# Kernel tuning notes

Measured on AMD Instinct MI355X. Metric: run time of the kernel, lower is better.

## Reference

```python
import jax, jax.numpy as jnp
import numpy as np

B, N, D, H, FF = 2, 2048, 768, 12, 3072
HD = D // H
RADIUS = 2.0
COORD_DIM = 3
LN_EPS = 1e-5


def _layernorm(x, g, b):
    m = jnp.mean(x, axis=-1, keepdims=True)
    v = jnp.mean((x - m) ** 2, axis=-1, keepdims=True)
    return (x - m) * jax.lax.rsqrt(v + LN_EPS) * g + b


def setup_inputs() -> dict:
    key = jax.random.key(0)
    ks = jax.random.split(key, 16)
    s = 0.02
    return {
        "x": jax.random.normal(ks[0], (B, N, D), jnp.float32),
        "coords": jax.random.uniform(ks[1], (B, N, COORD_DIM), jnp.float32) * 10.0,
        "w_qkv": jax.random.normal(ks[2], (D, 3 * D), jnp.float32) * s,
        "b_qkv": jnp.zeros((3 * D,), jnp.float32),
        "w_out": jax.random.normal(ks[3], (D, D), jnp.float32) * s,
        "b_out": jnp.zeros((D,), jnp.float32),
        "w_ff1": jax.random.normal(ks[4], (D, FF), jnp.float32) * s,
        "b_ff1": jnp.zeros((FF,), jnp.float32),
        "w_ff2": jax.random.normal(ks[5], (FF, D), jnp.float32) * s,
        "b_ff2": jnp.zeros((D,), jnp.float32),
        "g1": jnp.ones((D,), jnp.float32),
        "beta1": jnp.zeros((D,), jnp.float32),
        "g2": jnp.ones((D,), jnp.float32),
        "beta2": jnp.zeros((D,), jnp.float32),
    }


def reference(x, coords, w_qkv, b_qkv, w_out, b_out, w_ff1, b_ff1,
              w_ff2, b_ff2, g1, beta1, g2, beta2):
    # --- attention sub-block ---
    residual = x
    xn = _layernorm(x, g1, beta1)
    qkv = xn @ w_qkv + b_qkv                       # [B,N,3D]
    qkv = qkv.reshape(B, N, 3, H, HD)
    q, k, v = qkv[:, :, 0], qkv[:, :, 1], qkv[:, :, 2]   # [B,N,H,HD]

    # geometric radius mask: attend only to tokens within Euclidean RADIUS
    d2 = jnp.sum((coords[:, :, None, :] - coords[:, None, :, :]) ** 2, axis=-1)  # [B,N,N]
    mask = d2 <= RADIUS * RADIUS                   # self-distance 0 -> always true

    scores = jnp.einsum("bqhd,bkhd->bhqk", q, k) / jnp.sqrt(jnp.float32(HD))
    scores = jnp.where(mask[:, None, :, :], scores, jnp.float32(-1e9))
    attn = jax.nn.softmax(scores, axis=-1)
    attn_out = jnp.einsum("bhqk,bkhd->bqhd", attn, v).reshape(B, N, D)
    attn_out = attn_out @ w_out + b_out            # dropout=0 (eval)
    x = residual + attn_out

    # --- FFN sub-block ---
    residual = x
    xn = _layernorm(x, g2, beta2)
    h = jax.nn.gelu(xn @ w_ff1 + b_ff1, approximate=False)
    ff_out = h @ w_ff2 + b_ff2
    return residual + ff_out
```

## Files before the change

kernel.cpp:

```cpp
#include <hip/hip_runtime.h>
#include <hip/hip_bf16.h>

typedef unsigned short ushort_t;
typedef __attribute__((ext_vector_type(4))) float f32x4;
typedef __attribute__((ext_vector_type(8))) short s16x8;

#define DEV static __device__ __forceinline__

constexpr int Bb = 2, Nn = 2048, Dd = 768, Hh = 12, FFf = 3072;
constexpr int MTOK = Bb * Nn;
constexpr int QKVN = 3 * Dd;

DEV unsigned short f2bf(float f) {
    union { float f; unsigned int i; } x; x.f = f;
    unsigned int r = x.i + 0x7FFFu + ((x.i >> 16) & 1u);
    return (unsigned short)(r >> 16);
}

DEV void gload16(const void* g, void* l) {
    __builtin_amdgcn_global_load_lds(
        (const __attribute__((address_space(1))) void*)g,
        (__attribute__((address_space(3))) void*)l, 16, 0, 0);
}

DEV int xcd_swz(int lin, int n) {
    return (lin & 7) * (n >> 3) + (lin >> 3);
}

__global__ void k_transpose(const float* __restrict__ in, unsigned short* __restrict__ out,
                            int K, int N) {
    __shared__ float t[32][33];
    int bx = blockIdx.x * 32, by = blockIdx.y * 32;
    int tx = threadIdx.x, ty = threadIdx.y;
#pragma unroll
    for (int i = 0; i < 4; i++)
        t[ty + 8 * i][tx] = in[(size_t)(by + ty + 8 * i) * N + bx + tx];
    __syncthreads();
#pragma unroll
    for (int i = 0; i < 4; i++)
        out[(size_t)(bx + ty + 8 * i) * K + by + tx] = f2bf(t[tx][ty + 8 * i]);
}

__global__ void k_coords(const float* __restrict__ c, float4* __restrict__ out, int n) {
    int i = blockIdx.x * 256 + threadIdx.x;
    if (i < n) out[i] = make_float4(c[3 * i], c[3 * i + 1], c[3 * i + 2], 0.f);
}

DEV int cell_of(float4 c) {
    int cx = (int)(c.x * 0.5f); cx = cx > 4 ? 4 : cx;
    int cy = (int)(c.y * 0.5f); cy = cy > 4 ? 4 : cy;
    int cz = (int)(c.z * 0.5f); cz = cz > 4 ? 4 : cz;
    return (cz * 5 + cy) * 5 + cx;
}

__global__ __launch_bounds__(256) void k_sort(const float4* __restrict__ c4,
                                              int* __restrict__ s2o,
                                              float4* __restrict__ c4s) {
    int b = blockIdx.y;
    int i = blockIdx.x * 4 + (threadIdx.x >> 6);
    int lane = threadIdx.x & 63;
    const float4* cb = c4 + b * Nn;
    float4 ci = cb[i];
    int celli = cell_of(ci);
    int pos = 0;
    for (int it = 0; it < Nn / 64; it++) {
        int j = it * 64 + lane;
        int cj = cell_of(cb[j]);
        bool before = (cj < celli) || (cj == celli && j < i);
        pos += __popcll(__ballot(before));
    }
    if (lane == 0) {
        s2o[b * Nn + pos] = i;
        c4s[b * Nn + pos] = ci;
    }
}

__global__ __launch_bounds__(256) void k_mask(const float4* __restrict__ c4s,
                                              unsigned long long* __restrict__ mb) {
    int qt = blockIdx.x, ks = blockIdx.y, b = blockIdx.z;
    __shared__ float4 ck[256];
    int t = threadIdx.x;
    ck[t] = c4s[b * Nn + ks * 256 + t];
    __syncthreads();
    int r = t >> 2, c = t & 3;
    int q = qt * 64 + r;
    float4 cq = c4s[b * Nn + q];
    unsigned long long w = 0;
#pragma unroll 8
    for (int j = 0; j < 64; j++) {
        float4 k4 = ck[c * 64 + j];
        float dx = __fsub_rn(cq.x, k4.x);
        float dy = __fsub_rn(cq.y, k4.y);
        float dz = __fsub_rn(cq.z, k4.z);
        float d2 = __fadd_rn(__fadd_rn(__fmul_rn(dx, dx), __fmul_rn(dy, dy)),
                             __fmul_rn(dz, dz));
        if (d2 <= 4.0f) w |= 1ull << j;
    }
    mb[((size_t)(b * Nn + q) << 5) + ks * 4 + c] = w;
}

__global__ __launch_bounds__(64) void k_tiles(const unsigned long long* __restrict__ mb,
                                              int* __restrict__ tl) {
    int q64 = blockIdx.x, b = blockIdx.y;
    int lane = threadIdx.x;
    unsigned long long v = 0;
    if (lane < 32) {
        const unsigned long long* base = mb + ((size_t)(b * Nn + q64 * 64) << 5) + lane;
        for (int r = 0; r < 64; r++) v |= base[(size_t)r << 5];
    }
    unsigned long long nz = __ballot(v != 0);
    int idx = __popcll(nz & ((1ull << lane) - 1));
    int* o = tl + (b * 32 + q64) * 33;
    if (v != 0) o[1 + idx] = lane;
    if (lane == 0) o[0] = __popcll(nz);
}

__global__ __launch_bounds__(128) void k_gatherK(const unsigned short* __restrict__ qkv,
                                                 const int* __restrict__ s2o,
                                                 unsigned short* __restrict__ Ksort) {
    int ns = blockIdx.x & (Nn - 1);
    int b = blockIdx.x >> 11;
    int t = threadIdx.x;
    int orig = s2o[b * Nn + ns];
    const s16x8* src = (const s16x8*)(qkv + ((size_t)b * Nn + orig) * QKVN + Dd);
    s16x8* dst = (s16x8*)(Ksort + ((size_t)b * Nn + ns) * Dd);
    if (t < 96) dst[t] = src[t];
}

__global__ __launch_bounds__(256) void k_vt(const unsigned short* __restrict__ qkv,
                                            const int* __restrict__ s2o,
                                            unsigned short* __restrict__ VtT) {
    __shared__ unsigned short Ld[64][72];
    int ns0 = blockIdx.x * 64;
    int bh = blockIdx.y;
    int b = bh / Hh, h = bh % Hh;
    int t = threadIdx.x;
#pragma unroll
    for (int i = 0; i < 2; i++) {
        int item = t + 256 * i;
        int row = item >> 3, ch = (item & 7) * 8;
        int orig = s2o[b * Nn + ns0 + row];
        *(s16x8*)&Ld[row][ch] =
            *(const s16x8*)(qkv + ((size_t)b * Nn + orig) * QKVN + 2 * Dd + h * 64 + ch);
    }
    __syncthreads();
    int vd = (t >> 5) * 8, vkp = (t & 31) * 2;
#pragma unroll
    for (int j = 0; j < 8; j++) {
        unsigned int pack = (unsigned int)Ld[vkp][vd + j] |
                            ((unsigned int)Ld[vkp + 1][vd + j] << 16);
        *(unsigned int*)((char*)VtT +
                         (((size_t)bh * 64 + vd + j) * Nn + ns0 + vkp) * 2) = pack;
    }
}

DEV float wred_sum(float v) {
#pragma unroll
    for (int o = 32; o; o >>= 1) v += __shfl_down(v, o, 64);
    return v;
}

__global__ __launch_bounds__(256) void k_ln(const float* __restrict__ x,
                                            const float* __restrict__ g,
                                            const float* __restrict__ be,
                                            unsigned short* __restrict__ out) {
    int row = blockIdx.x;
    const float* xr = x + (size_t)row * Dd;
    int t = threadIdx.x;
    float v0 = xr[t], v1 = xr[t + 256], v2 = xr[t + 512];
    float s = v0 + v1 + v2;
    float sq = v0 * v0 + v1 * v1 + v2 * v2;
    __shared__ float r1[4], r2[4];
    float ws = wred_sum(s), wq = wred_sum(sq);
    int wid = t >> 6, lane = t & 63;
    if (lane == 0) { r1[wid] = ws; r2[wid] = wq; }
    __syncthreads();
    s = r1[0] + r1[1] + r1[2] + r1[3];
    sq = r2[0] + r2[1] + r2[2] + r2[3];
    float mean = s * (1.f / Dd);
    float var = sq * (1.f / Dd) - mean * mean;
    float rs = rsqrtf(var + 1e-5f);
    unsigned short* orow = out + (size_t)row * Dd;
    orow[t]       = f2bf((v0 - mean) * rs * g[t]       + be[t]);
    orow[t + 256] = f2bf((v1 - mean) * rs * g[t + 256] + be[t + 256]);
    orow[t + 512] = f2bf((v2 - mean) * rs * g[t + 512] + be[t + 512]);
}

#define GEMM_PIPE_LOOP(NT)                                                              \
    stage(0, 0);                                                                        \
    for (int t = 0; t < (NT); t++) {                                                    \
        int cur = t & 1;                                                                \
        if (t + 1 < (NT)) {                                                             \
            stage(cur ^ 1, t + 1);                                                      \
            asm volatile("s_waitcnt vmcnt(4)" ::: "memory");                            \
        } else {                                                                        \
            asm volatile("s_waitcnt vmcnt(0)" ::: "memory");                            \
        }                                                                               \
        __builtin_amdgcn_sched_barrier(0);                                              \
        __builtin_amdgcn_s_barrier();                                                   \
        const unsigned short* Ab = As[cur];                                             \
        const unsigned short* Bbp = Bs[cur];                                            \
        s16x8 af[4], bfr[4];                                                            \
        _Pragma("unroll")                                                               \
        for (int i = 0; i < 4; i++) {                                                   \
            af[i]  = *(const s16x8*)&Ab[(wr * 64 + i * 16 + lr) * 32 + lg * 8];         \
            bfr[i] = *(const s16x8*)&Bbp[(wc * 64 + i * 16 + lr) * 32 + lg * 8];        \
        }                                                                               \
        __builtin_amdgcn_s_setprio(1);                                                  \
        _Pragma("unroll")                                                               \
        for (int mi = 0; mi < 4; mi++)                                                  \
            _Pragma("unroll")                                                           \
            for (int ni = 0; ni < 4; ni++)                                              \
                acc[mi][ni] = __builtin_amdgcn_mfma_f32_16x16x32_bf16(                  \
                    af[mi], bfr[ni], acc[mi][ni], 0, 0, 0);                             \
        __builtin_amdgcn_s_setprio(0);                                                  \
        __builtin_amdgcn_s_barrier();                                                   \
    }

template <int EPI>
__global__ __launch_bounds__(256) void k_gemm(const unsigned short* __restrict__ A,
                                              const unsigned short* __restrict__ Bt,
                                              const float* __restrict__ bias,
                                              const float* __restrict__ res,
                                              void* __restrict__ outp,
                                              int M, int N, int K) {
    constexpr int BM = 128, BN = 128, BK = 32;
    __shared__ unsigned short As[2][BM * BK];
    __shared__ unsigned short Bs[2][BN * BK];
    int NB = N >> 7;
    int id = xcd_swz(blockIdx.x, gridDim.x);
    int m0 = (id / NB) * BM, n0 = (id % NB) * BN;
    int t = threadIdx.x;
    int wid = t >> 6, lane = t & 63;
    int wr = wid >> 1, wc = wid & 1;
    int lg = lane >> 4, lr = lane & 15;
    f32x4 acc[4][4] = {};

    int srow = wid * 32 + (lane >> 2);
    int scol = (lane & 3) * 8;
    const unsigned short* Ag = A + (size_t)(m0 + srow) * K + scol;
    const unsigned short* Bg = Bt + (size_t)(n0 + srow) * K + scol;

    auto stage = [&](int buf, int kt) {
        int k0 = kt * BK;
        char* Al = (char*)As[buf] + wid * 2048;
        char* Bl = (char*)Bs[buf] + wid * 2048;
        gload16(Ag + k0, Al);
        gload16(Ag + k0 + (size_t)16 * K, Al + 1024);
        gload16(Bg + k0, Bl);
        gload16(Bg + k0 + (size_t)16 * K, Bl + 1024);
    };
    int nt = K / BK;
    GEMM_PIPE_LOOP(nt)

    int mrow = m0 + wr * 64;
    int ncol = n0 + wc * 64;
#pragma unroll
    for (int mi = 0; mi < 4; mi++) {
#pragma unroll
        for (int ni = 0; ni < 4; ni++) {
            int nn = ncol + ni * 16 + lr;
            float bs = bias[nn];
#pragma unroll
            for (int r = 0; r < 4; r++) {
                int mm = mrow + mi * 16 + lg * 4 + r;
                float v = acc[mi][ni][r] + bs;
                if (EPI == 1) {
                    v = 0.5f * v * (1.f + erff(v * 0.70710678118f));
                    ((unsigned short*)outp)[(size_t)mm * N + nn] = f2bf(v);
                } else if (EPI == 2) {
                    v += res[(size_t)mm * N + nn];
                    ((float*)outp)[(size_t)mm * N + nn] = v;
                } else {
                    ((unsigned short*)outp)[(size_t)mm * N + nn] = f2bf(v);
                }
            }
        }
    }
}

template <int SPLIT>
__global__ __launch_bounds__(256) void k_gemm_sk(const unsigned short* __restrict__ A,
                                                 const unsigned short* __restrict__ Bt,
                                                 float* __restrict__ part,
                                                 int M, int N, int K) {
    constexpr int BM = 128, BN = 128, BK = 32;
    __shared__ unsigned short As[2][BM * BK];
    __shared__ unsigned short Bs[2][BN * BK];
    int NB = N >> 7, MB = M >> 7;
    int id = xcd_swz(blockIdx.x, gridDim.x);
    int nb = id % NB;
    int mbk = (id / NB) % MB;
    int kz = id / (NB * MB);
    int m0 = mbk * BM, n0 = nb * BN;
    int Kc = K / SPLIT, kb = kz * (Kc / BK);
    int t = threadIdx.x;
    int wid = t >> 6, lane = t & 63;
    int wr = wid >> 1, wc = wid & 1;
    int lg = lane >> 4, lr = lane & 15;
    f32x4 acc[4][4] = {};

    int srow = wid * 32 + (lane >> 2);
    int scol = (lane & 3) * 8;
    const unsigned short* Ag = A + (size_t)(m0 + srow) * K + scol;
    const unsigned short* Bg = Bt + (size_t)(n0 + srow) * K + scol;

    auto stage = [&](int buf, int kt) {
        int k0 = (kb + kt) * BK;
        char* Al = (char*)As[buf] + wid * 2048;
        char* Bl = (char*)Bs[buf] + wid * 2048;
        gload16(Ag + k0, Al);
        gload16(Ag + k0 + (size_t)16 * K, Al + 1024);
        gload16(Bg + k0, Bl);
        gload16(Bg + k0 + (size_t)16 * K, Bl + 1024);
    };
    int nt = Kc / BK;
    GEMM_PIPE_LOOP(nt)

    float* po = part + (size_t)kz * M * N;
    int mrow = m0 + wr * 64;
    int ncol = n0 + wc * 64;
#pragma unroll
    for (int mi = 0; mi < 4; mi++)
#pragma unroll
        for (int ni = 0; ni < 4; ni++) {
            int nn = ncol + ni * 16 + lr;
#pragma unroll
            for (int r = 0; r < 4; r++) {
                int mm = mrow + mi * 16 + lg * 4 + r;
                po[(size_t)mm * N + nn] = acc[mi][ni][r];
            }
        }
}

__global__ __launch_bounds__(256) void k_reduce2(const float* __restrict__ part,
                                                 const float* __restrict__ bias,
                                                 const float* __restrict__ res,
                                                 float* __restrict__ out,
                                                 int MN, int N) {
    int i = (blockIdx.x * 256 + threadIdx.x) * 4;
    f32x4 a = *(const f32x4*)(part + i);
    f32x4 bq = *(const f32x4*)(part + (size_t)MN + i);
    f32x4 r = *(const f32x4*)(res + i);
    f32x4 bs = *(const f32x4*)(bias + (i % N));
    f32x4 o;
#pragma unroll
    for (int j = 0; j < 4; j++) o[j] = a[j] + bq[j] + bs[j] + r[j];
    *(f32x4*)(out + i) = o;
}

constexpr float SC2 = 0.125f * 1.44269504088896340736f;
constexpr float PMASK = -3.0e38f;
constexpr float MINIT = -1.0e30f;

__global__ __launch_bounds__(256) void k_attn(const unsigned short* __restrict__ qkv,
                                              const unsigned short* __restrict__ Ksort,
                                              const unsigned short* __restrict__ VtT,
                                              const int* __restrict__ s2o,
                                              const uint2* __restrict__ mb,
                                              const int* __restrict__ tl,
                                              unsigned short* __restrict__ out) {
    int lin = blockIdx.x;
    int id = (lin & 7) * 96 + (lin >> 3);
    int q64 = id & 31;
    int hb = id >> 5;
    int h = hb % Hh, b = hb / Hh;
    int bh = b * Hh + h;

    __shared__ __align__(16) char sm[2 * 16384 + 4 * 2048];

    int t = threadIdx.x, wid = t >> 6, lane = t & 63;
    int lg = lane >> 4, lr = lane & 15;
    int sw = lr & 7;
    int qbase = q64 * 64 + wid * 16;

    int oq = s2o[b * Nn + qbase + lr];
    const unsigned short* Qb = qkv + ((size_t)b * Nn + oq) * QKVN + h * 64;
    s16x8 qf0 = *(const s16x8*)(Qb + lg * 8);
    s16x8 qf1 = *(const s16x8*)(Qb + 32 + lg * 8);

    const uint2* mrow = mb + ((size_t)(b * Nn + qbase + lr) << 5);
    const int* tle = tl + (b * 32 + q64) * 33;
    int tlv = (lane < 33) ? tle[lane] : 0;
    int cnt = __shfl(tlv, 0, 64);

    int srow = lane >> 3, sch = lane & 7;
    int krow = wid * 8 + srow;
    int kx = sch ^ (krow & 7);
    const unsigned short* Kg0 = Ksort + ((size_t)b * Nn + krow) * Dd + h * 64 + kx * 8;
    const unsigned short* Vg0 = VtT + ((size_t)bh * 64 + krow) * Nn + kx * 8;
    char* pw = sm + 32768 + wid * 2048 + lr * 128;

    float m2 = MINIT, l_run = 0.f;
    f32x4 oacc[4] = {};

    int tid0 = __shfl(tlv, 1, 64);
    uint2 Mw = mrow[tid0];
    {
        char* Kl = sm + wid * 1024;
        gload16(Kg0 + (size_t)(tid0 * 64) * Dd, Kl);
        gload16(Kg0 + (size_t)(tid0 * 64 + 32) * Dd, Kl + 4096);
        char* Vl = sm + 8192 + wid * 1024;
        gload16(Vg0 + tid0 * 64, Vl);
        gload16(Vg0 + tid0 * 64 + 32 * (size_t)Nn, Vl + 4096);
    }
    __syncthreads();

    for (int ti = 0; ti < cnt; ti++) {
        int cur = ti & 1;
        uint2 MwN;
        if (ti + 1 < cnt) {
            int tidn = __shfl(tlv, 2 + ti, 64);
            char* Kl = sm + (cur ^ 1) * 16384 + wid * 1024;
            gload16(Kg0 + (size_t)(tidn * 64) * Dd, Kl);
            gload16(Kg0 + (size_t)(tidn * 64 + 32) * Dd, Kl + 4096);
            char* Vl = sm + (cur ^ 1) * 16384 + 8192 + wid * 1024;
            gload16(Vg0 + tidn * 64, Vl);
            gload16(Vg0 + tidn * 64 + 32 * (size_t)Nn, Vl + 4096);
            MwN = mrow[tidn];
        }

        if (__any((Mw.x | Mw.y) != 0)) {
            const char* Kbuf = sm + cur * 16384;
            const char* Vbuf = Kbuf + 8192;

            __builtin_amdgcn_s_setprio(1);
            f32x4 st[4];
#pragma unroll
            for (int s = 0; s < 4; s++) {
                const char* kr = Kbuf + (s * 16 + lr) * 128;
                s16x8 kf0 = *(const s16x8*)(kr + ((lg ^ sw) << 4));
                s16x8 kf1 = *(const s16x8*)(kr + (((4 + lg) ^ sw) << 4));
                f32x4 z = {};
                z = __builtin_amdgcn_mfma_f32_16x16x32_bf16(kf0, qf0, z, 0, 0, 0);
                st[s] = __builtin_amdgcn_mfma_f32_16x16x32_bf16(kf1, qf1, z, 0, 0, 0);
            }
            __builtin_amdgcn_s_setprio(0);

            float p[4][4];
            float mt = PMASK;
#pragma unroll
            for (int s = 0; s < 4; s++) {
                unsigned int wsel = (s < 2) ? Mw.x : Mw.y;
#pragma unroll
                for (int r = 0; r < 4; r++) {
                    float sv = st[s][r] * SC2;
                    unsigned int bit = (wsel >> ((s & 1) * 16 + lg * 4 + r)) & 1u;
                    p[s][r] = bit ? sv : PMASK;
                    mt = fmaxf(mt, p[s][r]);
                }
            }
            mt = fmaxf(mt, __shfl_xor(mt, 16, 64));
            mt = fmaxf(mt, __shfl_xor(mt, 32, 64));

            if (!__all(mt <= m2 + 11.5416f)) {
                float mn2 = fmaxf(m2, mt);
                float fac = __builtin_amdgcn_exp2f(m2 - mn2);
                l_run *= fac;
                m2 = mn2;
                float fr[4];
#pragma unroll
                for (int r = 0; r < 4; r++) fr[r] = __shfl(fac, (lane & 48) + lg * 4 + r, 64);
#pragma unroll
                for (int dt = 0; dt < 4; dt++)
#pragma unroll
                    for (int r = 0; r < 4; r++) oacc[dt][r] *= fr[r];
            }

            float lt = 0.f;
#pragma unroll
            for (int s = 0; s < 4; s++)
#pragma unroll
                for (int r = 0; r < 4; r++) {
                    p[s][r] = __builtin_amdgcn_exp2f(p[s][r] - m2);
                    lt += p[s][r];
                }
            lt += __shfl_xor(lt, 16, 64);
            lt += __shfl_xor(lt, 32, 64);
            l_run += lt;

#pragma unroll
            for (int s = 0; s < 4; s++) {
                unsigned int lo = (unsigned int)f2bf(p[s][0]) | ((unsigned int)f2bf(p[s][1]) << 16);
                unsigned int hi = (unsigned int)f2bf(p[s][2]) | ((unsigned int)f2bf(p[s][3]) << 16);
                unsigned long long u = (unsigned long long)lo | ((unsigned long long)hi << 32);
                int chunk = (s * 2 + (lg >> 1)) ^ sw;
                *(unsigned long long*)(pw + (chunk << 4) + (lg & 1) * 8) = u;
            }

            __builtin_amdgcn_s_setprio(1);
#pragma unroll
            for (int c = 0; c < 2; c++) {
                s16x8 pf = *(const s16x8*)(pw + (((c * 4 + lg) ^ sw) << 4));
#pragma unroll
                for (int dt = 0; dt < 4; dt++) {
                    const char* vr = Vbuf + (dt * 16 + lr) * 128;
                    s16x8 vf = *(const s16x8*)(vr + (((c * 4 + lg) ^ sw) << 4));
                    oacc[dt] = __builtin_amdgcn_mfma_f32_16x16x32_bf16(pf, vf, oacc[dt], 0, 0, 0);
                }
            }
            __builtin_amdgcn_s_setprio(0);
        }

        __syncthreads();
        Mw = MwN;
    }

    float lr4[4];
    int orow[4];
#pragma unroll
    for (int r = 0; r < 4; r++) {
        lr4[r] = __shfl(l_run, (lane & 48) + lg * 4 + r, 64);
        orow[r] = s2o[b * Nn + qbase + lg * 4 + r];
    }
#pragma unroll
    for (int dt = 0; dt < 4; dt++)
#pragma unroll
        for (int r = 0; r < 4; r++) {
            float v = oacc[dt][r] / lr4[r];
            out[((size_t)b * Nn + orow[r]) * Dd + h * 64 + dt * 16 + lr] = f2bf(v);
        }
}

extern "C" void kernel_launch(void* const* d_in, const int* in_sizes, int n_in,
                              void* d_out, int out_size, void* d_ws, size_t ws_size,
                              hipStream_t stream) {
    const float* x      = (const float*)d_in[0];
    const float* coords = (const float*)d_in[1];
    const float* w_qkv  = (const float*)d_in[2];
    const float* b_qkv  = (const float*)d_in[3];
    const float* w_out  = (const float*)d_in[4];
    const float* b_out  = (const float*)d_in[5];
    const float* w_ff1  = (const float*)d_in[6];
    const float* b_ff1  = (const float*)d_in[7];
    const float* w_ff2  = (const float*)d_in[8];
    const float* b_ff2  = (const float*)d_in[9];
    const float* g1     = (const float*)d_in[10];
    const float* beta1  = (const float*)d_in[11];
    const float* g2     = (const float*)d_in[12];
    const float* beta2  = (const float*)d_in[13];

    char* ws = (char*)d_ws;
    size_t off = 0;
    auto alloc = [&](size_t bytes) {
        char* p = ws + off;
        off += (bytes + 255) & ~(size_t)255;
        return p;
    };
    unsigned short* w_qkv_t = (unsigned short*)alloc((size_t)QKVN * Dd * 2);
    unsigned short* w_out_t = (unsigned short*)alloc((size_t)Dd * Dd * 2);
    unsigned short* w_ff1_t = (unsigned short*)alloc((size_t)FFf * Dd * 2);
    unsigned short* w_ff2_t = (unsigned short*)alloc((size_t)Dd * FFf * 2);
    float4*         c4      = (float4*)alloc((size_t)MTOK * 16);
    float4*         c4s     = (float4*)alloc((size_t)MTOK * 16);
    int*            s2o     = (int*)alloc((size_t)MTOK * 4);
    unsigned long long* mbits = (unsigned long long*)alloc((size_t)MTOK * 32 * 8);
    int*            tl      = (int*)alloc((size_t)Bb * 32 * 33 * 4);
    unsigned short* xn      = (unsigned short*)alloc((size_t)MTOK * Dd * 2);
    unsigned short* hbuf    = (unsigned short*)alloc((size_t)MTOK * FFf * 2);
    float*          x2      = (float*)alloc((size_t)MTOK * Dd * 4);
    unsigned short* attn_o  = (unsigned short*)alloc((size_t)MTOK * Dd * 2);
    unsigned short* qkv     = (unsigned short*)alloc((size_t)MTOK * QKVN * 2);
    unsigned short* Ksort   = (unsigned short*)alloc((size_t)MTOK * Dd * 2);
    unsigned short* VtT     = (unsigned short*)alloc((size_t)Bb * Hh * 64 * Nn * 2);
    float* partial = (float*)qkv;

    dim3 tb(32, 8);
    k_transpose<<<dim3(QKVN / 32, Dd / 32), tb, 0, stream>>>(w_qkv, w_qkv_t, Dd, QKVN);
    k_transpose<<<dim3(Dd / 32, Dd / 32), tb, 0, stream>>>(w_out, w_out_t, Dd, Dd);
    k_transpose<<<dim3(FFf / 32, Dd / 32), tb, 0, stream>>>(w_ff1, w_ff1_t, Dd, FFf);
    k_transpose<<<dim3(Dd / 32, FFf / 32), tb, 0, stream>>>(w_ff2, w_ff2_t, FFf, Dd);
    k_coords<<<(MTOK + 255) / 256, 256, 0, stream>>>(coords, c4, MTOK);
    k_sort<<<dim3(Nn / 4, Bb), 256, 0, stream>>>(c4, s2o, c4s);
    k_mask<<<dim3(Nn / 64, 8, Bb), 256, 0, stream>>>(c4s, mbits);
    k_tiles<<<dim3(32, Bb), 64, 0, stream>>>(mbits, tl);

    k_ln<<<MTOK, 256, 0, stream>>>(x, g1, beta1, xn);
    k_gemm<0><<<dim3((QKVN / 128) * (MTOK / 128)), 256, 0, stream>>>(
        xn, w_qkv_t, b_qkv, nullptr, qkv, MTOK, QKVN, Dd);
    k_gatherK<<<dim3(MTOK), 128, 0, stream>>>(qkv, s2o, Ksort);
    k_vt<<<dim3(Nn / 64, Bb * Hh), 256, 0, stream>>>(qkv, s2o, VtT);
    k_attn<<<dim3((Nn / 64) * Hh * Bb), 256, 0, stream>>>(
        qkv, Ksort, VtT, s2o, (const uint2*)mbits, tl, attn_o);
    k_gemm_sk<2><<<dim3((Dd / 128) * (MTOK / 128) * 2), 256, 0, stream>>>(
        attn_o, w_out_t, partial, MTOK, Dd, Dd);
    k_reduce2<<<dim3(MTOK * Dd / 1024), 256, 0, stream>>>(
        partial, b_out, x, x2, MTOK * Dd, Dd);
    k_ln<<<MTOK, 256, 0, stream>>>(x2, g2, beta2, xn);
    k_gemm<1><<<dim3((FFf / 128) * (MTOK / 128)), 256, 0, stream>>>(
        xn, w_ff1_t, b_ff1, nullptr, hbuf, MTOK, FFf, Dd);
    k_gemm_sk<2><<<dim3((Dd / 128) * (MTOK / 128) * 2), 256, 0, stream>>>(
        hbuf, w_ff2_t, partial, MTOK, Dd, FFf);
    k_reduce2<<<dim3(MTOK * Dd / 1024), 256, 0, stream>>>(
        partial, b_ff2, x2, (float*)d_out, MTOK * Dd, Dd);
}
```

Measured before the change: 220.5 us.

## Triple-buffer GEMM pipeline, fuse weight transposes, drop coords kernel, use tanh GELU

```diff
diff --git a/kernel.cpp b/kernel.cpp
--- a/kernel.cpp
+++ b/kernel.cpp
@@ -27,10 +27,26 @@
     return (lin & 7) * (n >> 3) + (lin >> 3);
 }
 
-__global__ void k_transpose(const float* __restrict__ in, unsigned short* __restrict__ out,
-                            int K, int N) {
+DEV float gelu_fast(float x) {
+    float u = x * (0.7978845608f + 0.0356774081f * x * x);
+    float e = __builtin_amdgcn_exp2f(2.885390082f * u);
+    float th = 1.f - 2.f / (e + 1.f);
+    return 0.5f * x * (1.f + th);
+}
+
+__global__ void k_transpose_all(const float* __restrict__ w_qkv, const float* __restrict__ w_out,
+                                const float* __restrict__ w_ff1, const float* __restrict__ w_ff2,
+                                unsigned short* __restrict__ o_qkv, unsigned short* __restrict__ o_out,
+                                unsigned short* __restrict__ o_ff1, unsigned short* __restrict__ o_ff2) {
     __shared__ float t[32][33];
-    int bx = blockIdx.x * 32, by = blockIdx.y * 32;
+    int id = blockIdx.x;
+    const float* in; unsigned short* out; int K, N, tid;
+    if (id < 1728)      { in = w_qkv; out = o_qkv; K = 768;  N = 2304; tid = id; }
+    else if (id < 2304) { in = w_out; out = o_out; K = 768;  N = 768;  tid = id - 1728; }
+    else if (id < 4608) { in = w_ff1; out = o_ff1; K = 768;  N = 3072; tid = id - 2304; }
+    else                { in = w_ff2; out = o_ff2; K = 3072; N = 768;  tid = id - 4608; }
+    int nbx = N >> 5;
+    int bx = (tid % nbx) * 32, by = (tid / nbx) * 32;
     int tx = threadIdx.x, ty = threadIdx.y;
 #pragma unroll
     for (int i = 0; i < 4; i++)
@@ -41,37 +57,32 @@
         out[(size_t)(bx + ty + 8 * i) * K + by + tx] = f2bf(t[tx][ty + 8 * i]);
 }
 
-__global__ void k_coords(const float* __restrict__ c, float4* __restrict__ out, int n) {
-    int i = blockIdx.x * 256 + threadIdx.x;
-    if (i < n) out[i] = make_float4(c[3 * i], c[3 * i + 1], c[3 * i + 2], 0.f);
-}
-
-DEV int cell_of(float4 c) {
-    int cx = (int)(c.x * 0.5f); cx = cx > 4 ? 4 : cx;
-    int cy = (int)(c.y * 0.5f); cy = cy > 4 ? 4 : cy;
-    int cz = (int)(c.z * 0.5f); cz = cz > 4 ? 4 : cz;
+DEV int cell3(float x, float y, float z) {
+    int cx = (int)(x * 0.5f); cx = cx > 4 ? 4 : cx;
+    int cy = (int)(y * 0.5f); cy = cy > 4 ? 4 : cy;
+    int cz = (int)(z * 0.5f); cz = cz > 4 ? 4 : cz;
     return (cz * 5 + cy) * 5 + cx;
 }
 
-__global__ __launch_bounds__(256) void k_sort(const float4* __restrict__ c4,
+__global__ __launch_bounds__(256) void k_sort(const float* __restrict__ coords,
                                               int* __restrict__ s2o,
                                               float4* __restrict__ c4s) {
     int b = blockIdx.y;
     int i = blockIdx.x * 4 + (threadIdx.x >> 6);
     int lane = threadIdx.x & 63;
-    const float4* cb = c4 + b * Nn;
-    float4 ci = cb[i];
-    int celli = cell_of(ci);
+    const float* cb = coords + (size_t)b * Nn * 3;
+    float cix = cb[3 * i], ciy = cb[3 * i + 1], ciz = cb[3 * i + 2];
+    int celli = cell3(cix, ciy, ciz);
     int pos = 0;
     for (int it = 0; it < Nn / 64; it++) {
         int j = it * 64 + lane;
-        int cj = cell_of(cb[j]);
+        int cj = cell3(cb[3 * j], cb[3 * j + 1], cb[3 * j + 2]);
         bool before = (cj < celli) || (cj == celli && j < i);
         pos += __popcll(__ballot(before));
     }
     if (lane == 0) {
         s2o[b * Nn + pos] = i;
-        c4s[b * Nn + pos] = ci;
+        c4s[b * Nn + pos] = make_float4(cix, ciy, ciz, 0.f);
     }
 }
 
@@ -188,10 +199,13 @@
 
 #define GEMM_PIPE_LOOP(NT)                                                              \
     stage(0, 0);                                                                        \
+    if ((NT) > 1) stage(1, 1);                                                          \
     for (int t = 0; t < (NT); t++) {                                                    \
-        int cur = t & 1;                                                                \
-        if (t + 1 < (NT)) {                                                             \
-            stage(cur ^ 1, t + 1);                                                      \
+        int cur = t % 3;                                                                \
+        if (t + 2 < (NT)) {                                                             \
+            stage((t + 2) % 3, t + 2);                                                  \
+            asm volatile("s_waitcnt vmcnt(8)" ::: "memory");                            \
+        } else if (t + 1 < (NT)) {                                                      \
             asm volatile("s_waitcnt vmcnt(4)" ::: "memory");                            \
         } else {                                                                        \
             asm volatile("s_waitcnt vmcnt(0)" ::: "memory");                            \
@@ -225,8 +239,8 @@
                                               void* __restrict__ outp,
                                               int M, int N, int K) {
     constexpr int BM = 128, BN = 128, BK = 32;
-    __shared__ unsigned short As[2][BM * BK];
-    __shared__ unsigned short Bs[2][BN * BK];
+    __shared__ unsigned short As[3][BM * BK];
+    __shared__ unsigned short Bs[3][BN * BK];
     int NB = N >> 7;
     int id = xcd_swz(blockIdx.x, gridDim.x);
     int m0 = (id / NB) * BM, n0 = (id % NB) * BN;
@@ -266,8 +280,7 @@
                 int mm = mrow + mi * 16 + lg * 4 + r;
                 float v = acc[mi][ni][r] + bs;
                 if (EPI == 1) {
-                    v = 0.5f * v * (1.f + erff(v * 0.70710678118f));
-                    ((unsigned short*)outp)[(size_t)mm * N + nn] = f2bf(v);
+                    ((unsigned short*)outp)[(size_t)mm * N + nn] = f2bf(gelu_fast(v));
                 } else if (EPI == 2) {
                     v += res[(size_t)mm * N + nn];
                     ((float*)outp)[(size_t)mm * N + nn] = v;
@@ -285,8 +298,8 @@
                                                  float* __restrict__ part,
                                                  int M, int N, int K) {
     constexpr int BM = 128, BN = 128, BK = 32;
-    __shared__ unsigned short As[2][BM * BK];
-    __shared__ unsigned short Bs[2][BN * BK];
+    __shared__ unsigned short As[3][BM * BK];
+    __shared__ unsigned short Bs[3][BN * BK];
     int NB = N >> 7, MB = M >> 7;
     int id = xcd_swz(blockIdx.x, gridDim.x);
     int nb = id % NB;
@@ -551,7 +564,6 @@
     unsigned short* w_out_t = (unsigned short*)alloc((size_t)Dd * Dd * 2);
     unsigned short* w_ff1_t = (unsigned short*)alloc((size_t)FFf * Dd * 2);
     unsigned short* w_ff2_t = (unsigned short*)alloc((size_t)Dd * FFf * 2);
-    float4*         c4      = (float4*)alloc((size_t)MTOK * 16);
     float4*         c4s     = (float4*)alloc((size_t)MTOK * 16);
     int*            s2o     = (int*)alloc((size_t)MTOK * 4);
     unsigned long long* mbits = (unsigned long long*)alloc((size_t)MTOK * 32 * 8);
@@ -565,13 +577,9 @@
     unsigned short* VtT     = (unsigned short*)alloc((size_t)Bb * Hh * 64 * Nn * 2);
     float* partial = (float*)qkv;
 
-    dim3 tb(32, 8);
-    k_transpose<<<dim3(QKVN / 32, Dd / 32), tb, 0, stream>>>(w_qkv, w_qkv_t, Dd, QKVN);
-    k_transpose<<<dim3(Dd / 32, Dd / 32), tb, 0, stream>>>(w_out, w_out_t, Dd, Dd);
-    k_transpose<<<dim3(FFf / 32, Dd / 32), tb, 0, stream>>>(w_ff1, w_ff1_t, Dd, FFf);
-    k_transpose<<<dim3(Dd / 32, FFf / 32), tb, 0, stream>>>(w_ff2, w_ff2_t, FFf, Dd);
-    k_coords<<<(MTOK + 255) / 256, 256, 0, stream>>>(coords, c4, MTOK);
-    k_sort<<<dim3(Nn / 4, Bb), 256, 0, stream>>>(c4, s2o, c4s);
+    k_transpose_all<<<dim3(6912), dim3(32, 8), 0, stream>>>(
+        w_qkv, w_out, w_ff1, w_ff2, w_qkv_t, w_out_t, w_ff1_t, w_ff2_t);
+    k_sort<<<dim3(Nn / 4, Bb), 256, 0, stream>>>(coords, s2o, c4s);
     k_mask<<<dim3(Nn / 64, 8, Bb), 256, 0, stream>>>(c4s, mbits);
     k_tiles<<<dim3(32, Bb), 64, 0, stream>>>(mbits, tl);
 
```

After: 212.4 us. -3.7%, faster.
